# Kernel optimization log

Measured on AMD Instinct MI355X. Metric: run time of the kernel, lower is better.

## Reference

```python
import jax, jax.numpy as jnp
import numpy as np

B, S, HID = 2, 1024, 4096
NH, NKV = 32, 8            # query heads, kv heads (GQA)
D = HID // NH              # head_size = 128
G = NH // NKV              # groups = 4
SCALE = D ** -0.5


def setup_inputs() -> dict:
    key = jax.random.key(0)
    k1, k2, k3 = jax.random.split(key, 3)
    hidden_states = jax.random.normal(k1, (B, S, HID), dtype=jnp.float32)
    # rotary tables: dim=head_size, base=10000 (PositionRotaryEmbedding.static)
    inv_freq = 1.0 / (10000.0 ** (jnp.arange(0, D, 2, dtype=jnp.float32) / D))  # [D/2]
    t = jnp.arange(S, dtype=jnp.float32)
    freqs = jnp.outer(t, inv_freq)                       # [S, D/2]
    cos, sin = jnp.cos(freqs), jnp.sin(freqs)
    wqkv = jax.random.normal(k2, (HID, (NH + 2 * NKV) * D), dtype=jnp.float32) * (HID ** -0.5)
    wo = jax.random.normal(k3, (NH * D, HID), dtype=jnp.float32) * (HID ** -0.5)
    return {"hidden_states": hidden_states, "cos": cos, "sin": sin, "wqkv": wqkv, "wo": wo}


def _rope(x, cos, sin):
    # interleaved-pair rotary (TGI convention); x: [B,S,H,D], cos/sin: [S,D/2]
    x1, x2 = x[..., 0::2], x[..., 1::2]
    c = cos[None, :, None, :]
    s = sin[None, :, None, :]
    r1 = x1 * c - x2 * s
    r2 = x1 * s + x2 * c
    return jnp.stack([r1, r2], axis=-1).reshape(x.shape)


def reference(hidden_states, cos, sin, wqkv, wo):
    qkv = hidden_states @ wqkv                                  # [B,S,(NH+2*NKV)*D]
    q = qkv[..., : NH * D].reshape(B, S, NH, D)
    k = qkv[..., NH * D : (NH + NKV) * D].reshape(B, S, NKV, D)
    v = qkv[..., (NH + NKV) * D :].reshape(B, S, NKV, D)
    q = _rope(q, cos, sin)
    k = _rope(k, cos, sin)
    # GQA: group query heads over kv heads
    qg = q.reshape(B, S, NKV, G, D)
    scores = jnp.einsum('bqkgd,bskd->bkgqs', qg, k) * SCALE     # [B,NKV,G,S,S]
    causal = jnp.tril(jnp.ones((S, S), dtype=bool))
    scores = jnp.where(causal, scores, jnp.finfo(scores.dtype).min)
    p = jax.nn.softmax(scores, axis=-1)
    out = jnp.einsum('bkgqs,bskd->bqkgd', p, v).reshape(B, S, NH * D)
    return out @ wo                                             # [B,S,HID]
```

## Files before the change

### kernel.cpp

```cpp
#include <hip/hip_runtime.h>
#include <hip/hip_bf16.h>

typedef __bf16 bf16;
typedef __attribute__((ext_vector_type(2))) __bf16 bf16x2;
typedef __attribute__((ext_vector_type(4))) __bf16 bf16x4;
typedef __attribute__((ext_vector_type(8))) __bf16 bf16x8;
typedef __attribute__((ext_vector_type(4))) float f32x4;

#define NB 2
#define SEQ 1024
#define HIDN 4096
#define NH 32
#define NKV 8
#define DH 128
#define QKV_N 6144
static constexpr float SCALE = 0.08838834764831845f;

#define MFMA(a, b, c) __builtin_amdgcn_mfma_f32_16x16x32_bf16((a), (b), (c), 0, 0, 0)

__device__ __forceinline__ void async16(const void* g, void* l) {
  __builtin_amdgcn_global_load_lds(
      (const __attribute__((address_space(1))) unsigned int*)g,
      (__attribute__((address_space(3))) unsigned int*)l,
      16, 0, 0);
}

__device__ __forceinline__ void barrier_raw() {
  asm volatile("" ::: "memory");
  __builtin_amdgcn_s_barrier();
  asm volatile("" ::: "memory");
}
#define VMCNT(n) asm volatile("s_waitcnt vmcnt(" #n ")" ::: "memory")
#define LGKM0 asm volatile("s_waitcnt lgkmcnt(0)" ::: "memory")

__global__ __launch_bounds__(256) void cvt_f32_bf16(const float* __restrict__ src,
                                                    bf16* __restrict__ dst, int n4) {
  int i = blockIdx.x * 256 + threadIdx.x;
  if (i >= n4) return;
  const float4 v = ((const float4*)src)[i];
  bf16x4 o = {(bf16)v.x, (bf16)v.y, (bf16)v.z, (bf16)v.w};
  ((bf16x4*)dst)[i] = o;
}

__global__ __launch_bounds__(256) void transpose_cvt(const float* __restrict__ src,
                                                     bf16* __restrict__ dst, int R, int C) {
  __shared__ float tl[32][33];
  const int j0 = blockIdx.x * 32, i0 = blockIdx.y * 32;
  const int tr = threadIdx.x >> 5, tc = threadIdx.x & 31;
#pragma unroll
  for (int p = 0; p < 4; ++p)
    tl[tr + p * 8][tc] = src[(size_t)(i0 + tr + p * 8) * C + j0 + tc];
  __syncthreads();
#pragma unroll
  for (int p = 0; p < 4; ++p)
    dst[(size_t)(j0 + tr + p * 8) * R + i0 + tc] = (bf16)tl[tc][tr + p * 8];
}

template <int BN, int OUT_BF16>
__global__ __launch_bounds__(512, 2) void gemm_dp2(const bf16* __restrict__ A,
                                                   const bf16* __restrict__ BT,
                                                   void* __restrict__ Cout,
                                                   int N, int K) {
  extern __shared__ char smem[];
  constexpr int CA = 128 * 32 * 2;
  constexpr int CB = BN * 32 * 2;
  constexpr int BUF = CA + CB;
  constexpr int LTOT = 1 + BN / 128;
  constexpr int FN = BN / 64;
  const int t = threadIdx.x, lane = t & 63, w = t >> 6;
  const int l16 = lane & 15, lq = lane >> 4;
  const int wm = w >> 2, wn = w & 3;

  const int nwg = gridDim.x;
  const int lin = ((int)blockIdx.x & 7) * (nwg >> 3) + ((int)blockIdx.x >> 3);
  const int m0 = (lin & 15) * 128;
  const int n0 = (lin >> 4) * BN;

  const int sslot = (t & 3) ^ ((t >> 3) & 3);
  const bf16* gsrc[LTOT];
  gsrc[0] = A + (size_t)(m0 + (t >> 2)) * K + sslot * 8;
#pragma unroll
  for (int u = 1; u < LTOT; ++u)
    gsrc[u] = BT + (size_t)(n0 + (u - 1) * 128 + (t >> 2)) * K + sslot * 8;

  int abyte[4], bbyte[FN];
#pragma unroll
  for (int f = 0; f < 4; ++f) {
    const int r = wm * 64 + f * 16 + l16;
    abyte[f] = r * 64 + ((lq ^ ((r >> 1) & 3)) << 4);
  }
#pragma unroll
  for (int j = 0; j < FN; ++j) {
    const int r = wn * (BN / 4) + j * 16 + l16;
    bbyte[j] = CA + r * 64 + ((lq ^ ((r >> 1) & 3)) << 4);
  }

  auto stage = [&](int kt) {
    char* d = smem + (kt & 3) * BUF + t * 16;
#pragma unroll
    for (int u = 0; u < LTOT; ++u) async16(gsrc[u] + (size_t)kt * 32, d + u * 8192);
  };
  auto ldfrag = [&](int kt, bf16x8(&a)[4], bf16x8(&b)[FN]) {
    const char* buf = smem + (kt & 3) * BUF;
#pragma unroll
    for (int f = 0; f < 4; ++f) a[f] = *(const bf16x8*)(buf + abyte[f]);
#pragma unroll
    for (int j = 0; j < FN; ++j) b[j] = *(const bf16x8*)(buf + bbyte[j]);
  };

  f32x4 acc[4][FN] = {};
  const int NT = K >> 5;

  bf16x8 a0[4], a1[4], b0[FN], b1[FN];

  stage(0);
  stage(1);
  stage(2);
  if constexpr (LTOT == 4) { VMCNT(8); } else { VMCNT(6); }
  barrier_raw();
  ldfrag(0, a0, b0);

  auto tilestep = [&](int kt, bf16x8(&aC)[4], bf16x8(&bC)[FN], bf16x8(&aN)[4],
                      bf16x8(&bN)[FN]) {
    if (kt + 3 < NT) {
      stage(kt + 3);
      if constexpr (LTOT == 4) { VMCNT(8); } else { VMCNT(6); }
    } else if (kt + 2 < NT) {
      if constexpr (LTOT == 4) { VMCNT(4); } else { VMCNT(3); }
    } else if (kt + 1 < NT) {
      VMCNT(0);
    }
    LGKM0;
    barrier_raw();
    if (kt + 1 < NT) ldfrag(kt + 1, aN, bN);
    __builtin_amdgcn_s_setprio(1);
#pragma unroll
    for (int f = 0; f < 4; ++f)
#pragma unroll
      for (int j = 0; j < FN; ++j) acc[f][j] = MFMA(aC[f], bC[j], acc[f][j]);
    __builtin_amdgcn_s_setprio(0);
  };

  for (int kt = 0; kt < NT; kt += 2) {
    tilestep(kt, a0, b0, a1, b1);
    tilestep(kt + 1, a1, b1, a0, b0);
  }

#pragma unroll
  for (int f = 0; f < 4; ++f)
#pragma unroll
    for (int j = 0; j < FN; ++j)
#pragma unroll
      for (int r = 0; r < 4; ++r) {
        const int row = m0 + wm * 64 + f * 16 + lq * 4 + r;
        const int col = n0 + wn * (BN / 4) + j * 16 + l16;
        if (OUT_BF16)
          ((bf16*)Cout)[(size_t)row * N + col] = (bf16)acc[f][j][r];
        else
          ((float*)Cout)[(size_t)row * N + col] = acc[f][j][r];
      }
}

__global__ __launch_bounds__(256) void rope_reshape(const bf16* __restrict__ qkv,
                                                    const float* __restrict__ cosp,
                                                    const float* __restrict__ sinp,
                                                    bf16* __restrict__ Qo,
                                                    bf16* __restrict__ Ko,
                                                    bf16* __restrict__ VTo) {
  const int row = blockIdx.x;
  const int b = row >> 10, s = row & 1023;
  const bf16* src = qkv + (size_t)row * QKV_N;
  for (int p = threadIdx.x; p < QKV_N / 2; p += 256) {
    const int col = p * 2;
    bf16x2 x = *(const bf16x2*)&src[col];
    const float x1 = (float)x.x, x2 = (float)x.y;
    if (col < 4096) {
      const int h = col >> 7, d = col & 127, i = (col & 127) >> 1;
      const float c = cosp[s * 64 + i], sn = sinp[s * 64 + i];
      bf16x2 o = {(bf16)((x1 * c - x2 * sn) * SCALE), (bf16)((x1 * sn + x2 * c) * SCALE)};
      *(bf16x2*)&Qo[((size_t)(b * NH + h) * SEQ + s) * DH + d] = o;
    } else if (col < 5120) {
      const int idx = col - 4096;
      const int kvh = idx >> 7, d = idx & 127, i = (idx & 127) >> 1;
      const float c = cosp[s * 64 + i], sn = sinp[s * 64 + i];
      bf16x2 o = {(bf16)(x1 * c - x2 * sn), (bf16)(x1 * sn + x2 * c)};
      *(bf16x2*)&Ko[((size_t)(b * NKV + kvh) * SEQ + s) * DH + d] = o;
    } else {
      const int idx = col - 5120;
      const int kvh = idx >> 7, d = idx & 127;
      bf16* vbase = VTo + ((size_t)(b * NKV + kvh) * DH + d) * SEQ + s;
      vbase[0] = x.x;
      vbase[SEQ] = x.y;
    }
  }
}

__global__ __launch_bounds__(512, 2) void flash_attn(const bf16* __restrict__ Q,
                                                     const bf16* __restrict__ K,
                                                     const bf16* __restrict__ VT,
                                                     bf16* __restrict__ O) {
  extern __shared__ char smem[];
  const int t = threadIdx.x, lane = t & 63, w = t >> 6;
  const int l16 = lane & 15, lq = lane >> 4;
  const int p = blockIdx.x;
  const int b = p >> 7, h = (p >> 2) & 31, Tb = p & 3;
  const int kvh = h >> 2;

  const bf16* Qb = Q + (size_t)(b * NH + h) * SEQ * DH;
  const bf16* Kb = K + (size_t)(b * NKV + kvh) * SEQ * DH;
  const bf16* Vb = VT + (size_t)(b * NKV + kvh) * DH * SEQ;

  const int qrA = Tb * 128 + w * 16;
  const int qrB = (7 - Tb) * 128 + w * 16;
  const int nAw = (qrA >> 6) + 1;
  const int nBw = (qrB >> 6) + 1;
  const int NT = 16 - 2 * Tb;

  bf16* plw = (bf16*)(smem + 98304) + w * (2 * 16 * 72);

  const bf16* kSrc = Kb + (size_t)(t >> 4) * DH + 8 * ((t & 15) ^ ((t >> 4) & 7));
  const bf16* vSrc = Vb + (size_t)(t >> 3) * SEQ + 8 * ((t & 7) ^ ((t >> 3) & 7));

  auto stage = [&](int kv) {
    char* bufb = smem + (kv % 3) * 32768;
    async16(kSrc + (size_t)(kv * 64) * DH, bufb + t * 16);
    async16(kSrc + (size_t)(kv * 64 + 32) * DH, bufb + 8192 + t * 16);
    async16(vSrc + kv * 64, bufb + 16384 + t * 16);
    async16(vSrc + (size_t)64 * SEQ + kv * 64, bufb + 24576 + t * 16);
  };

  int KX[4], VX[2];
#pragma unroll
  for (int kk = 0; kk < 4; ++kk) KX[kk] = ((kk * 4 + lq) ^ (l16 & 7)) << 4;
#pragma unroll
  for (int c = 0; c < 2; ++c) VX[c] = ((c * 4 + lq) ^ (l16 & 7)) << 4;

  bf16x8 qfA[4], qfB[4];
#pragma unroll
  for (int kk = 0; kk < 4; ++kk) {
    qfA[kk] = *(const bf16x8*)&Qb[(size_t)(qrA + l16) * DH + kk * 32 + lq * 8];
    qfB[kk] = *(const bf16x8*)&Qb[(size_t)(qrB + l16) * DH + kk * 32 + lq * 8];
  }

  f32x4 accA[8] = {}, accB[8] = {};
  float mA[4], lA[4], mB[4], lB[4];
#pragma unroll
  for (int r = 0; r < 4; ++r) {
    mA[r] = mB[r] = -INFINITY;
    lA[r] = lB[r] = 0.f;
  }

  auto finish = [&](f32x4(&s)[4], float(&m)[4], float(&l)[4], f32x4(&acc)[8], int slot,
                    bool mask, int kv, int qr) {
    if (mask) {
#pragma unroll
      for (int nt = 0; nt < 4; ++nt)
#pragma unroll
        for (int r = 0; r < 4; ++r)
          if (kv * 64 + nt * 16 + l16 > qr + lq * 4 + r) s[nt][r] = -INFINITY;
    }
#pragma unroll
    for (int r = 0; r < 4; ++r) {
      float mx = fmaxf(fmaxf(s[0][r], s[1][r]), fmaxf(s[2][r], s[3][r]));
#pragma unroll
      for (int off = 1; off < 16; off <<= 1) mx = fmaxf(mx, __shfl_xor(mx, off));
      const float mn = fmaxf(m[r], mx);
      const float corr = __expf(m[r] - mn);
      m[r] = mn;
      float ps = 0.f;
#pragma unroll
      for (int nt = 0; nt < 4; ++nt) {
        const float pv = __expf(s[nt][r] - mn);
        s[nt][r] = pv;
        ps += pv;
      }
#pragma unroll
      for (int off = 1; off < 16; off <<= 1) ps += __shfl_xor(ps, off);
      l[r] = l[r] * corr + ps;
#pragma unroll
      for (int j = 0; j < 8; ++j) acc[j][r] *= corr;
    }
#pragma unroll
    for (int nt = 0; nt < 4; ++nt)
#pragma unroll
      for (int r = 0; r < 4; ++r)
        plw[slot * 1152 + (lq * 4 + r) * 72 + nt * 16 + l16] = (bf16)s[nt][r];
  };

  stage(0);
  stage(1);
  VMCNT(4);
  barrier_raw();

  for (int kv = 0; kv < NT; ++kv) {
    const char* kbuf = smem + (kv % 3) * 32768;
    const char* vbuf = kbuf + 16384;
    if (kv + 2 < NT) stage(kv + 2);

    if (kv < nAw) {
      f32x4 sA[4] = {}, sB[4] = {};
      __builtin_amdgcn_s_setprio(1);
#pragma unroll
      for (int nt = 0; nt < 4; ++nt) {
        const char* kr = kbuf + (nt * 16 + l16) * 256;
        bf16x8 k0 = *(const bf16x8*)(kr + KX[0]);
        bf16x8 k1 = *(const bf16x8*)(kr + KX[1]);
        bf16x8 k2 = *(const bf16x8*)(kr + KX[2]);
        bf16x8 k3 = *(const bf16x8*)(kr + KX[3]);
        sA[nt] = MFMA(qfA[0], k0, sA[nt]);
        sB[nt] = MFMA(qfB[0], k0, sB[nt]);
        sA[nt] = MFMA(qfA[1], k1, sA[nt]);
        sB[nt] = MFMA(qfB[1], k1, sB[nt]);
        sA[nt] = MFMA(qfA[2], k2, sA[nt]);
        sB[nt] = MFMA(qfB[2], k2, sB[nt]);
        sA[nt] = MFMA(qfA[3], k3, sA[nt]);
        sB[nt] = MFMA(qfB[3], k3, sB[nt]);
      }
      __builtin_amdgcn_s_setprio(0);
      finish(sA, mA, lA, accA, 0, kv == nAw - 1, kv, qrA);
      finish(sB, mB, lB, accB, 1, kv == nBw - 1, kv, qrB);
      bf16x8 pA0 = *(const bf16x8*)&plw[l16 * 72 + lq * 8];
      bf16x8 pA1 = *(const bf16x8*)&plw[l16 * 72 + 32 + lq * 8];
      bf16x8 pB0 = *(const bf16x8*)&plw[1152 + l16 * 72 + lq * 8];
      bf16x8 pB1 = *(const bf16x8*)&plw[1152 + l16 * 72 + 32 + lq * 8];
      __builtin_amdgcn_s_setprio(1);
#pragma unroll
      for (int j = 0; j < 8; ++j) {
        const char* vr = vbuf + (j * 16 + l16) * 128;
        bf16x8 v0 = *(const bf16x8*)(vr + VX[0]);
        bf16x8 v1 = *(const bf16x8*)(vr + VX[1]);
        accA[j] = MFMA(pA0, v0, accA[j]);
        accB[j] = MFMA(pB0, v0, accB[j]);
        accA[j] = MFMA(pA1, v1, accA[j]);
        accB[j] = MFMA(pB1, v1, accB[j]);
      }
      __builtin_amdgcn_s_setprio(0);
    } else if (kv < nBw) {
      f32x4 sB[4] = {};
      __builtin_amdgcn_s_setprio(1);
#pragma unroll
      for (int nt = 0; nt < 4; ++nt) {
        const char* kr = kbuf + (nt * 16 + l16) * 256;
        bf16x8 k0 = *(const bf16x8*)(kr + KX[0]);
        bf16x8 k1 = *(const bf16x8*)(kr + KX[1]);
        bf16x8 k2 = *(const bf16x8*)(kr + KX[2]);
        bf16x8 k3 = *(const bf16x8*)(kr + KX[3]);
        sB[nt] = MFMA(qfB[0], k0, sB[nt]);
        sB[nt] = MFMA(qfB[1], k1, sB[nt]);
        sB[nt] = MFMA(qfB[2], k2, sB[nt]);
        sB[nt] = MFMA(qfB[3], k3, sB[nt]);
      }
      __builtin_amdgcn_s_setprio(0);
      finish(sB, mB, lB, accB, 1, kv == nBw - 1, kv, qrB);
      bf16x8 pB0 = *(const bf16x8*)&plw[1152 + l16 * 72 + lq * 8];
      bf16x8 pB1 = *(const bf16x8*)&plw[1152 + l16 * 72 + 32 + lq * 8];
      __builtin_amdgcn_s_setprio(1);
#pragma unroll
      for (int j = 0; j < 8; ++j) {
        const char* vr = vbuf + (j * 16 + l16) * 128;
        bf16x8 v0 = *(const bf16x8*)(vr + VX[0]);
        bf16x8 v1 = *(const bf16x8*)(vr + VX[1]);
        accB[j] = MFMA(pB0, v0, accB[j]);
        accB[j] = MFMA(pB1, v1, accB[j]);
      }
      __builtin_amdgcn_s_setprio(0);
    }

    if (kv + 2 < NT) { VMCNT(4); } else { VMCNT(0); }
    barrier_raw();
  }

  auto wout = [&](f32x4(&acc)[8], float(&l)[4], int qr) {
#pragma unroll
    for (int r = 0; r < 4; ++r) {
      const float inv = 1.f / l[r];
      const size_t orow = ((size_t)b * SEQ + qr + lq * 4 + r) * HIDN + h * DH;
#pragma unroll
      for (int j = 0; j < 8; ++j) O[orow + j * 16 + l16] = (bf16)(acc[j][r] * inv);
    }
  };
  wout(accA, lA, qrA);
  wout(accB, lB, qrB);
}

extern "C" void kernel_launch(void* const* d_in, const int* in_sizes, int n_in,
                              void* d_out, int out_size, void* d_ws, size_t ws_size,
                              hipStream_t stream) {
  const float* hidden = (const float*)d_in[0];
  const float* cosp = (const float*)d_in[1];
  const float* sinp = (const float*)d_in[2];
  const float* wqkv = (const float*)d_in[3];
  const float* wo = (const float*)d_in[4];
  float* out = (float*)d_out;

  char* ws = (char*)d_ws;
  bf16* hiddenB = (bf16*)(ws);
  bf16* wqkvT  = (bf16*)(ws + 16777216);
  bf16* woT    = (bf16*)(ws + 67108864);
  bf16* qkvB   = (bf16*)(ws + 100663296);
  bf16* Qb     = (bf16*)(ws + 125829120);
  bf16* Kb     = (bf16*)(ws + 142606336);
  bf16* VTb    = (bf16*)(ws + 146800640);
  bf16* attnB  = hiddenB;

  cvt_f32_bf16<<<8192, 256, 0, stream>>>(hidden, hiddenB, 2097152);
  transpose_cvt<<<dim3(192, 128), 256, 0, stream>>>(wqkv, wqkvT, 4096, 6144);
  transpose_cvt<<<dim3(128, 128), 256, 0, stream>>>(wo, woT, 4096, 4096);
  gemm_dp2<384, 1><<<dim3(256), 512, 131072, stream>>>(hiddenB, wqkvT, qkvB, 6144, 4096);
  rope_reshape<<<2048, 256, 0, stream>>>(qkvB, cosp, sinp, Qb, Kb, VTb);
  flash_attn<<<dim3(256), 512, 135168, stream>>>(Qb, Kb, VTb, attnB);
  gemm_dp2<256, 0><<<dim3(256), 512, 98304, stream>>>(attnB, woT, out, 4096, 4096);
}
```

Measured before the change: 300.3 us.

## Replace GEMM with simpler 3-stage single-buffer-fragment kernel at higher occupancy

Replaces the register double-buffered 4-stage GEMM with a simpler kernel. It uses a 128x256 tile, a 3-stage LDS ring (72KB) and launch bounds allowing 4 blocks per CU. The QKV projection now runs 384 blocks with BN=256 instead of 256 blocks with BN=384. The aim is to get latency hiding from occupancy rather than explicit fragment prefetch, but MFMA now waits on LDS reads each step and the LDS budget may not actually fit 4 blocks.

```diff
diff --git a/kernel.cpp b/kernel.cpp
--- a/kernel.cpp
+++ b/kernel.cpp
@@ -31,7 +31,6 @@
   asm volatile("" ::: "memory");
 }
 #define VMCNT(n) asm volatile("s_waitcnt vmcnt(" #n ")" ::: "memory")
-#define LGKM0 asm volatile("s_waitcnt lgkmcnt(0)" ::: "memory")
 
 __global__ __launch_bounds__(256) void cvt_f32_bf16(const float* __restrict__ src,
                                                     bf16* __restrict__ dst, int n4) {
@@ -56,104 +55,81 @@
     dst[(size_t)(j0 + tr + p * 8) * R + i0 + tc] = (bf16)tl[tc][tr + p * 8];
 }
 
-template <int BN, int OUT_BF16>
-__global__ __launch_bounds__(512, 2) void gemm_dp2(const bf16* __restrict__ A,
-                                                   const bf16* __restrict__ BT,
-                                                   void* __restrict__ Cout,
-                                                   int N, int K) {
+template <int OUT_BF16>
+__global__ __launch_bounds__(512, 4) void gemm_s(const bf16* __restrict__ A,
+                                                 const bf16* __restrict__ BT,
+                                                 void* __restrict__ Cout,
+                                                 int N, int K, int nbm) {
   extern __shared__ char smem[];
-  constexpr int CA = 128 * 32 * 2;
-  constexpr int CB = BN * 32 * 2;
-  constexpr int BUF = CA + CB;
-  constexpr int LTOT = 1 + BN / 128;
-  constexpr int FN = BN / 64;
+  constexpr int BUF = 24576;
   const int t = threadIdx.x, lane = t & 63, w = t >> 6;
   const int l16 = lane & 15, lq = lane >> 4;
   const int wm = w >> 2, wn = w & 3;
 
   const int nwg = gridDim.x;
   const int lin = ((int)blockIdx.x & 7) * (nwg >> 3) + ((int)blockIdx.x >> 3);
-  const int m0 = (lin & 15) * 128;
-  const int n0 = (lin >> 4) * BN;
+  const int m0 = (lin % nbm) * 128;
+  const int n0 = (lin / nbm) * 256;
 
   const int sslot = (t & 3) ^ ((t >> 3) & 3);
-  const bf16* gsrc[LTOT];
-  gsrc[0] = A + (size_t)(m0 + (t >> 2)) * K + sslot * 8;
-#pragma unroll
-  for (int u = 1; u < LTOT; ++u)
-    gsrc[u] = BT + (size_t)(n0 + (u - 1) * 128 + (t >> 2)) * K + sslot * 8;
-
-  int abyte[4], bbyte[FN];
+  const bf16* g0 = A + (size_t)(m0 + (t >> 2)) * K + sslot * 8;
+  const bf16* g1 = BT + (size_t)(n0 + (t >> 2)) * K + sslot * 8;
+  const bf16* g2 = BT + (size_t)(n0 + 128 + (t >> 2)) * K + sslot * 8;
+
+  int abyte[4], bbyte[4];
 #pragma unroll
   for (int f = 0; f < 4; ++f) {
-    const int r = wm * 64 + f * 16 + l16;
-    abyte[f] = r * 64 + ((lq ^ ((r >> 1) & 3)) << 4);
-  }
-#pragma unroll
-  for (int j = 0; j < FN; ++j) {
-    const int r = wn * (BN / 4) + j * 16 + l16;
-    bbyte[j] = CA + r * 64 + ((lq ^ ((r >> 1) & 3)) << 4);
+    const int ra = wm * 64 + f * 16 + l16;
+    abyte[f] = ra * 64 + ((lq ^ ((ra >> 1) & 3)) << 4);
+    const int rb = wn * 64 + f * 16 + l16;
+    bbyte[f] = 8192 + rb * 64 + ((lq ^ ((rb >> 1) & 3)) << 4);
   }
 
   auto stage = [&](int kt) {
-    char* d = smem + (kt & 3) * BUF + t * 16;
-#pragma unroll
-    for (int u = 0; u < LTOT; ++u) async16(gsrc[u] + (size_t)kt * 32, d + u * 8192);
+    char* d = smem + (kt % 3) * BUF + t * 16;
+    async16(g0 + (size_t)kt * 32, d);
+    async16(g1 + (size_t)kt * 32, d + 8192);
+    async16(g2 + (size_t)kt * 32, d + 16384);
   };
-  auto ldfrag = [&](int kt, bf16x8(&a)[4], bf16x8(&b)[FN]) {
-    const char* buf = smem + (kt & 3) * BUF;
-#pragma unroll
-    for (int f = 0; f < 4; ++f) a[f] = *(const bf16x8*)(buf + abyte[f]);
-#pragma unroll
-    for (int j = 0; j < FN; ++j) b[j] = *(const bf16x8*)(buf + bbyte[j]);
-  };
-
-  f32x4 acc[4][FN] = {};
+
+  f32x4 acc[4][4] = {};
   const int NT = K >> 5;
-
-  bf16x8 a0[4], a1[4], b0[FN], b1[FN];
 
   stage(0);
   stage(1);
-  stage(2);
-  if constexpr (LTOT == 4) { VMCNT(8); } else { VMCNT(6); }
+  VMCNT(3);
   barrier_raw();
-  ldfrag(0, a0, b0);
-
-  auto tilestep = [&](int kt, bf16x8(&aC)[4], bf16x8(&bC)[FN], bf16x8(&aN)[4],
-                      bf16x8(&bN)[FN]) {
-    if (kt + 3 < NT) {
-      stage(kt + 3);
-      if constexpr (LTOT == 4) { VMCNT(8); } else { VMCNT(6); }
-    } else if (kt + 2 < NT) {
-      if constexpr (LTOT == 4) { VMCNT(4); } else { VMCNT(3); }
+
+  for (int kt = 0; kt < NT; ++kt) {
+    const char* buf = smem + (kt % 3) * BUF;
+    bf16x8 af[4], bfr[4];
+#pragma unroll
+    for (int f = 0; f < 4; ++f) af[f] = *(const bf16x8*)(buf + abyte[f]);
+#pragma unroll
+    for (int j = 0; j < 4; ++j) bfr[j] = *(const bf16x8*)(buf + bbyte[j]);
+    if (kt + 2 < NT) {
+      stage(kt + 2);
+      VMCNT(3);
     } else if (kt + 1 < NT) {
       VMCNT(0);
     }
-    LGKM0;
     barrier_raw();
-    if (kt + 1 < NT) ldfrag(kt + 1, aN, bN);
     __builtin_amdgcn_s_setprio(1);
 #pragma unroll
     for (int f = 0; f < 4; ++f)
 #pragma unroll
-      for (int j = 0; j < FN; ++j) acc[f][j] = MFMA(aC[f], bC[j], acc[f][j]);
+      for (int j = 0; j < 4; ++j) acc[f][j] = MFMA(af[f], bfr[j], acc[f][j]);
     __builtin_amdgcn_s_setprio(0);
-  };
-
-  for (int kt = 0; kt < NT; kt += 2) {
-    tilestep(kt, a0, b0, a1, b1);
-    tilestep(kt + 1, a1, b1, a0, b0);
   }
 
 #pragma unroll
   for (int f = 0; f < 4; ++f)
 #pragma unroll
-    for (int j = 0; j < FN; ++j)
+    for (int j = 0; j < 4; ++j)
 #pragma unroll
       for (int r = 0; r < 4; ++r) {
         const int row = m0 + wm * 64 + f * 16 + lq * 4 + r;
-        const int col = n0 + wn * (BN / 4) + j * 16 + l16;
+        const int col = n0 + wn * 64 + j * 16 + l16;
         if (OUT_BF16)
           ((bf16*)Cout)[(size_t)row * N + col] = (bf16)acc[f][j][r];
         else
@@ -406,8 +382,8 @@
   cvt_f32_bf16<<<8192, 256, 0, stream>>>(hidden, hiddenB, 2097152);
   transpose_cvt<<<dim3(192, 128), 256, 0, stream>>>(wqkv, wqkvT, 4096, 6144);
   transpose_cvt<<<dim3(128, 128), 256, 0, stream>>>(wo, woT, 4096, 4096);
-  gemm_dp2<384, 1><<<dim3(256), 512, 131072, stream>>>(hiddenB, wqkvT, qkvB, 6144, 4096);
+  gemm_s<1><<<dim3(384), 512, 73728, stream>>>(hiddenB, wqkvT, qkvB, 6144, 4096, 16);
   rope_reshape<<<2048, 256, 0, stream>>>(qkvB, cosp, sinp, Qb, Kb, VTb);
   flash_attn<<<dim3(256), 512, 135168, stream>>>(Qb, Kb, VTb, attnB);
-  gemm_dp2<256, 0><<<dim3(256), 512, 98304, stream>>>(attnB, woT, out, 4096, 4096);
-}
+  gemm_s<0><<<dim3(256), 512, 73728, stream>>>(attnB, woT, out, 4096, 4096, 16);
+}
```

Measured after the change: 320.0 us. 6.6% more time.

## Restructure GEMMs to 4-wave blocks with smaller tiles and triple-buffered pipeline

Applied to the files above, without the earlier changes.

Replaces the 8-wave, 4-stage, register-double-buffered GEMM with a 4-wave kernel that uses narrower N tiles (192 for the QKV projection, 128 for the output projection), 3 LDS stages, and fragment loads taken directly from LDS each step. Grids double to 512 blocks and LDS per block drops, so more blocks can be resident per CU. The cost is less prefetch depth and no register-level overlap of LDS reads with MFMA, which may expose latency.

```diff
diff --git a/kernel.cpp b/kernel.cpp
--- a/kernel.cpp
+++ b/kernel.cpp
@@ -31,7 +31,6 @@
   asm volatile("" ::: "memory");
 }
 #define VMCNT(n) asm volatile("s_waitcnt vmcnt(" #n ")" ::: "memory")
-#define LGKM0 asm volatile("s_waitcnt lgkmcnt(0)" ::: "memory")
 
 __global__ __launch_bounds__(256) void cvt_f32_bf16(const float* __restrict__ src,
                                                     bf16* __restrict__ dst, int n4) {
@@ -57,7 +56,7 @@
 }
 
 template <int BN, int OUT_BF16>
-__global__ __launch_bounds__(512, 2) void gemm_dp2(const bf16* __restrict__ A,
+__global__ __launch_bounds__(256, 2) void gemm_cr2(const bf16* __restrict__ A,
                                                    const bf16* __restrict__ BT,
                                                    void* __restrict__ Cout,
                                                    int N, int K) {
@@ -65,23 +64,25 @@
   constexpr int CA = 128 * 32 * 2;
   constexpr int CB = BN * 32 * 2;
   constexpr int BUF = CA + CB;
-  constexpr int LTOT = 1 + BN / 128;
-  constexpr int FN = BN / 64;
+  constexpr int LU = 2 + BN / 64;
+  constexpr int FN = BN / 32;
   const int t = threadIdx.x, lane = t & 63, w = t >> 6;
   const int l16 = lane & 15, lq = lane >> 4;
-  const int wm = w >> 2, wn = w & 3;
+  const int wm = w >> 1, wn = w & 1;
 
   const int nwg = gridDim.x;
   const int lin = ((int)blockIdx.x & 7) * (nwg >> 3) + ((int)blockIdx.x >> 3);
   const int m0 = (lin & 15) * 128;
   const int n0 = (lin >> 4) * BN;
 
+  const int srow = t >> 2;
   const int sslot = (t & 3) ^ ((t >> 3) & 3);
-  const bf16* gsrc[LTOT];
-  gsrc[0] = A + (size_t)(m0 + (t >> 2)) * K + sslot * 8;
-#pragma unroll
-  for (int u = 1; u < LTOT; ++u)
-    gsrc[u] = BT + (size_t)(n0 + (u - 1) * 128 + (t >> 2)) * K + sslot * 8;
+  const bf16* gsrc[LU];
+  gsrc[0] = A + (size_t)(m0 + srow) * K + sslot * 8;
+  gsrc[1] = A + (size_t)(m0 + 64 + srow) * K + sslot * 8;
+#pragma unroll
+  for (int u = 2; u < LU; ++u)
+    gsrc[u] = BT + (size_t)(n0 + (u - 2) * 64 + srow) * K + sslot * 8;
 
   int abyte[4], bbyte[FN];
 #pragma unroll
@@ -91,59 +92,44 @@
   }
 #pragma unroll
   for (int j = 0; j < FN; ++j) {
-    const int r = wn * (BN / 4) + j * 16 + l16;
+    const int r = wn * (BN / 2) + j * 16 + l16;
     bbyte[j] = CA + r * 64 + ((lq ^ ((r >> 1) & 3)) << 4);
   }
 
   auto stage = [&](int kt) {
-    char* d = smem + (kt & 3) * BUF + t * 16;
-#pragma unroll
-    for (int u = 0; u < LTOT; ++u) async16(gsrc[u] + (size_t)kt * 32, d + u * 8192);
-  };
-  auto ldfrag = [&](int kt, bf16x8(&a)[4], bf16x8(&b)[FN]) {
-    const char* buf = smem + (kt & 3) * BUF;
-#pragma unroll
-    for (int f = 0; f < 4; ++f) a[f] = *(const bf16x8*)(buf + abyte[f]);
-#pragma unroll
-    for (int j = 0; j < FN; ++j) b[j] = *(const bf16x8*)(buf + bbyte[j]);
+    char* d = smem + (kt % 3) * BUF + t * 16;
+#pragma unroll
+    for (int u = 0; u < LU; ++u) async16(gsrc[u] + (size_t)kt * 32, d + u * 4096);
   };
 
   f32x4 acc[4][FN] = {};
   const int NT = K >> 5;
 
-  bf16x8 a0[4], a1[4], b0[FN], b1[FN];
-
   stage(0);
   stage(1);
-  stage(2);
-  if constexpr (LTOT == 4) { VMCNT(8); } else { VMCNT(6); }
+  if constexpr (BN == 192) { VMCNT(5); } else { VMCNT(4); }
   barrier_raw();
-  ldfrag(0, a0, b0);
-
-  auto tilestep = [&](int kt, bf16x8(&aC)[4], bf16x8(&bC)[FN], bf16x8(&aN)[4],
-                      bf16x8(&bN)[FN]) {
-    if (kt + 3 < NT) {
-      stage(kt + 3);
-      if constexpr (LTOT == 4) { VMCNT(8); } else { VMCNT(6); }
-    } else if (kt + 2 < NT) {
-      if constexpr (LTOT == 4) { VMCNT(4); } else { VMCNT(3); }
+
+  for (int kt = 0; kt < NT; ++kt) {
+    const char* buf = smem + (kt % 3) * BUF;
+    bf16x8 af[4], bfr[FN];
+#pragma unroll
+    for (int f = 0; f < 4; ++f) af[f] = *(const bf16x8*)(buf + abyte[f]);
+#pragma unroll
+    for (int j = 0; j < FN; ++j) bfr[j] = *(const bf16x8*)(buf + bbyte[j]);
+    if (kt + 2 < NT) {
+      stage(kt + 2);
+      if constexpr (BN == 192) { VMCNT(5); } else { VMCNT(4); }
     } else if (kt + 1 < NT) {
       VMCNT(0);
     }
-    LGKM0;
     barrier_raw();
-    if (kt + 1 < NT) ldfrag(kt + 1, aN, bN);
     __builtin_amdgcn_s_setprio(1);
 #pragma unroll
     for (int f = 0; f < 4; ++f)
 #pragma unroll
-      for (int j = 0; j < FN; ++j) acc[f][j] = MFMA(aC[f], bC[j], acc[f][j]);
+      for (int j = 0; j < FN; ++j) acc[f][j] = MFMA(af[f], bfr[j], acc[f][j]);
     __builtin_amdgcn_s_setprio(0);
-  };
-
-  for (int kt = 0; kt < NT; kt += 2) {
-    tilestep(kt, a0, b0, a1, b1);
-    tilestep(kt + 1, a1, b1, a0, b0);
   }
 
 #pragma unroll
@@ -153,7 +139,7 @@
 #pragma unroll
       for (int r = 0; r < 4; ++r) {
         const int row = m0 + wm * 64 + f * 16 + lq * 4 + r;
-        const int col = n0 + wn * (BN / 4) + j * 16 + l16;
+        const int col = n0 + wn * (BN / 2) + j * 16 + l16;
         if (OUT_BF16)
           ((bf16*)Cout)[(size_t)row * N + col] = (bf16)acc[f][j][r];
         else
@@ -406,8 +392,8 @@
   cvt_f32_bf16<<<8192, 256, 0, stream>>>(hidden, hiddenB, 2097152);
   transpose_cvt<<<dim3(192, 128), 256, 0, stream>>>(wqkv, wqkvT, 4096, 6144);
   transpose_cvt<<<dim3(128, 128), 256, 0, stream>>>(wo, woT, 4096, 4096);
-  gemm_dp2<384, 1><<<dim3(256), 512, 131072, stream>>>(hiddenB, wqkvT, qkvB, 6144, 4096);
+  gemm_cr2<192, 1><<<dim3(512), 256, 61440, stream>>>(hiddenB, wqkvT, qkvB, 6144, 4096);
   rope_reshape<<<2048, 256, 0, stream>>>(qkvB, cosp, sinp, Qb, Kb, VTb);
   flash_attn<<<dim3(256), 512, 135168, stream>>>(Qb, Kb, VTb, attnB);
-  gemm_dp2<256, 0><<<dim3(256), 512, 98304, stream>>>(attnB, woT, out, 4096, 4096);
-}
+  gemm_cr2<128, 0><<<dim3(512), 256, 49152, stream>>>(attnB, woT, out, 4096, 4096);
+}
```

New measurement: 317.7 us. 5.8% more time.
